# Optimization experiments

Measured on AMD Instinct MI355X. Metric: run time of the kernel, lower is better.

Reference implementation:

```python
import jax, jax.numpy as jnp
import numpy as np

N_NODES = 100000
N_EDGES = 1600000
N_GRAPHS = 512
IN_FEATS = 128
HIDDEN = 128
EXTRA = 8


def setup_inputs() -> dict:
    key = jax.random.key(0)
    ks = jax.random.split(key, 20)
    inp = {
        'feats_node': jax.random.normal(ks[0], (N_NODES, IN_FEATS), jnp.float32),
        'feats_graph': jax.random.normal(ks[1], (N_GRAPHS, EXTRA), jnp.float32),
        'edge_src': jax.random.randint(ks[2], (N_EDGES,), 0, N_NODES, jnp.int32),
        'edge_dst': jax.random.randint(ks[3], (N_EDGES,), 0, N_NODES, jnp.int32),
        'graph_ids': jnp.sort(jax.random.randint(ks[4], (N_NODES,), 0, N_GRAPHS, jnp.int32)),
        # GraphConv weights (in, out) and biases, init ~ N(0, 0.5^2) / zeros as in torch code
        'W1': 0.5 * jax.random.normal(ks[5], (IN_FEATS, HIDDEN), jnp.float32),
        'b1': jnp.zeros((HIDDEN,), jnp.float32),
        'W2': 0.5 * jax.random.normal(ks[6], (HIDDEN, HIDDEN), jnp.float32),
        'b2': jnp.zeros((HIDDEN,), jnp.float32),
        'W3': 0.5 * jax.random.normal(ks[7], (HIDDEN, HIDDEN), jnp.float32),
        'b3': jnp.zeros((HIDDEN,), jnp.float32),
        # MLP head
        'Wl1': 0.5 * jax.random.normal(ks[8], (HIDDEN + EXTRA, 2 * HIDDEN), jnp.float32),
        'bl1': jnp.zeros((2 * HIDDEN,), jnp.float32),
        'Wl2': 0.5 * jax.random.normal(ks[9], (2 * HIDDEN, HIDDEN), jnp.float32),
        'bl2': jnp.zeros((HIDDEN,), jnp.float32),
        'Wl3': 0.5 * jax.random.normal(ks[10], (HIDDEN, 1), jnp.float32),
        'bl3': jnp.zeros((1,), jnp.float32),
    }
    return inp


def _graph_conv(x, edge_src, edge_dst, norm_src, norm_dst, W, b):
    # DGL GraphConv, norm='both': D_dst^{-1/2} A D_src^{-1/2} X W + b
    h = x * norm_src[:, None]
    agg = jax.ops.segment_sum(h[edge_src], edge_dst, num_segments=N_NODES)
    agg = agg * norm_dst[:, None]
    return agg @ W + b


def reference(feats_node, feats_graph, edge_src, edge_dst, graph_ids,
              W1, b1, W2, b2, W3, b3, Wl1, bl1, Wl2, bl2, Wl3, bl3):
    ones_e = jnp.ones((N_EDGES,), jnp.float32)
    deg_out = jax.ops.segment_sum(ones_e, edge_src, num_segments=N_NODES)
    deg_in = jax.ops.segment_sum(ones_e, edge_dst, num_segments=N_NODES)
    norm_src = jnp.clip(deg_out, 1.0) ** -0.5  # out-degree norm on source side
    norm_dst = jnp.clip(deg_in, 1.0) ** -0.5   # in-degree norm on dest side

    x = jax.nn.selu(_graph_conv(feats_node, edge_src, edge_dst, norm_src, norm_dst, W1, b1))
    x = jax.nn.selu(_graph_conv(x, edge_src, edge_dst, norm_src, norm_dst, W2, b2))
    x = _graph_conv(x, edge_src, edge_dst, norm_src, norm_dst, W3, b3)

    # segment-mean readout per graph
    sums = jax.ops.segment_sum(x, graph_ids, num_segments=N_GRAPHS)
    counts = jax.ops.segment_sum(jnp.ones((N_NODES,), jnp.float32), graph_ids, num_segments=N_GRAPHS)
    embedding = sums / jnp.clip(counts, 1.0)[:, None]

    y = jnp.concatenate([embedding, feats_graph], axis=1)
    y = jax.nn.selu(y @ Wl1 + bl1)
    y = jax.nn.selu(y @ Wl2 + bl2)
    return (y @ Wl3 + bl3).reshape(-1)
```

## Files before the change

kernel.cpp:

```cpp
#include <hip/hip_runtime.h>
#include <hip/hip_fp16.h>
#include <math.h>

#define N_NODES   100000
#define N_EDGES   1600000
#define N_GRAPHS  512
#define FEAT      128
#define EXTRA     8

#define NB    196
#define CAPB  10240
#define PA_T  3072
#define PA_K  12

typedef _Float16 half8_t __attribute__((ext_vector_type(8)));
typedef float    f32x4_t __attribute__((ext_vector_type(4)));

static __device__ __forceinline__ float selu_f(float x){
    const float alpha = 1.6732632423543772f;
    const float scale = 1.0507009873554805f;
    return scale * (x > 0.0f ? x : alpha * expm1f(x));
}

__global__ void k_initcur(int* __restrict__ gcursor, int* __restrict__ scursor){
    int i = threadIdx.x;
    if (i < NB){ gcursor[i] = i*CAPB; scursor[i] = i*CAPB; }
}

__global__ __launch_bounds__(256) void k_passA2(
        const int* __restrict__ esrc, const int* __restrict__ edst,
        int* __restrict__ gcursor, int* __restrict__ scursor,
        unsigned* __restrict__ tmp, ushort* __restrict__ tmp2){
    __shared__ int      lcount[NB];
    __shared__ int      lscan[256];
    __shared__ int      gbase[NB];
    __shared__ ushort   bid[PA_T];
    __shared__ unsigned staged[PA_T];
    __shared__ int      Vtot;
    int t = threadIdx.x;
    int base = blockIdx.x * PA_T;

    unsigned ed[PA_K], es[PA_K]; int valid[PA_K];
    #pragma unroll
    for (int k = 0; k < PA_K; ++k){
        int e = base + k*256 + t;
        valid[k] = (e < N_EDGES);
        ed[k] = valid[k] ? (unsigned)edst[e] : 0u;
        es[k] = valid[k] ? (unsigned)esrc[e] : 0u;
    }

    for (int i = t; i < NB; i += 256) lcount[i] = 0;
    __syncthreads();
    int bk[PA_K], slot[PA_K];
    #pragma unroll
    for (int k = 0; k < PA_K; ++k){
        if (valid[k]){
            bk[k] = (int)(ed[k] >> 9);
            slot[k] = atomicAdd(&lcount[bk[k]], 1);
        } else bk[k] = -1;
    }
    __syncthreads();
    int v = (t < NB) ? lcount[t] : 0;
    lscan[t] = v;
    __syncthreads();
    for (int d = 1; d < 256; d <<= 1){
        int u = (t >= d) ? lscan[t-d] : 0;
        __syncthreads();
        lscan[t] += u;
        __syncthreads();
    }
    int excl = lscan[t] - v;
    if (t < NB) gbase[t] = atomicAdd(&gcursor[t], v);
    __syncthreads();
    lscan[t] = excl;
    if (t == 255) Vtot = excl + v;
    __syncthreads();
    #pragma unroll
    for (int k = 0; k < PA_K; ++k){
        if (bk[k] >= 0){
            int i = lscan[bk[k]] + slot[k];
            staged[i] = (ed[k] & 511u) | (es[k] << 9);
            bid[i] = (ushort)bk[k];
        }
    }
    __syncthreads();
    {
        int total = Vtot;
        for (int i = t; i < total; i += 256){
            int b = bid[i];
            tmp[gbase[b] + (i - lscan[b])] = staged[i];
        }
    }
    __syncthreads();

    ushort* sstag = (ushort*)staged;
    for (int i = t; i < NB; i += 256) lcount[i] = 0;
    __syncthreads();
    #pragma unroll
    for (int k = 0; k < PA_K; ++k){
        if (valid[k]){
            bk[k] = (int)(es[k] >> 9);
            slot[k] = atomicAdd(&lcount[bk[k]], 1);
        } else bk[k] = -1;
    }
    __syncthreads();
    v = (t < NB) ? lcount[t] : 0;
    lscan[t] = v;
    __syncthreads();
    for (int d = 1; d < 256; d <<= 1){
        int u = (t >= d) ? lscan[t-d] : 0;
        __syncthreads();
        lscan[t] += u;
        __syncthreads();
    }
    excl = lscan[t] - v;
    if (t < NB) gbase[t] = atomicAdd(&scursor[t], v);
    __syncthreads();
    lscan[t] = excl;
    if (t == 255) Vtot = excl + v;
    __syncthreads();
    #pragma unroll
    for (int k = 0; k < PA_K; ++k){
        if (bk[k] >= 0){
            int i = lscan[bk[k]] + slot[k];
            sstag[i] = (ushort)(es[k] & 511u);
            bid[i] = (ushort)bk[k];
        }
    }
    __syncthreads();
    {
        int total = Vtot;
        for (int i = t; i < total; i += 256){
            int b = bid[i];
            tmp2[gbase[b] + (i - lscan[b])] = sstag[i];
        }
    }
}

__global__ __launch_bounds__(256) void k_srchist(
        const ushort* __restrict__ tmp2, const int* __restrict__ scursor,
        float* __restrict__ ns){
    __shared__ int hc[512];
    int b = blockIdx.x, t = threadIdx.x;
    int node0 = b << 9;
    int lo = b*CAPB;
    int hi = scursor[b]; if (hi > lo + CAPB) hi = lo + CAPB;
    hc[t] = 0; hc[t+256] = 0;
    __syncthreads();
    for (int p = lo + t; p < hi; p += 256)
        atomicAdd(&hc[tmp2[p]], 1);
    __syncthreads();
    int n0 = node0 + t, n1 = n0 + 256;
    if (n0 < N_NODES){ int c = hc[t];     ns[n0] = rsqrtf((float)(c > 1 ? c : 1)); }
    if (n1 < N_NODES){ int c = hc[t+256]; ns[n1] = rsqrtf((float)(c > 1 ? c : 1)); }
}

__global__ __launch_bounds__(256) void k_passB(
        const unsigned* __restrict__ tmp, const int* __restrict__ gcursor,
        int* __restrict__ row_beg, int* __restrict__ row_end,
        int* __restrict__ col, float* __restrict__ nd){
    __shared__ int hc[512];
    __shared__ int hs[512];
    int b = blockIdx.x, t = threadIdx.x;
    int node0 = b << 9;
    int lo = b*CAPB;
    int hi = gcursor[b]; if (hi > lo + CAPB) hi = lo + CAPB;
    hc[t] = 0; hc[t+256] = 0;
    __syncthreads();
    for (int p = lo + t; p < hi; p += 256)
        atomicAdd(&hc[tmp[p] & 511u], 1);
    __syncthreads();
    int a0 = hc[2*t], a1 = hc[2*t+1];
    int s = a0 + a1;
    hs[t] = s;
    __syncthreads();
    for (int d = 1; d < 256; d <<= 1){
        int u = (t >= d) ? hs[t-d] : 0;
        __syncthreads();
        hs[t] += u;
        __syncthreads();
    }
    int excl = hs[t] - s;
    __syncthreads();
    hs[2*t]   = excl;
    hs[2*t+1] = excl + a0;
    int n0 = node0 + 2*t, n1 = n0 + 1;
    if (n0 < N_NODES){
        row_beg[n0] = lo + excl;
        row_end[n0] = lo + excl + a0;
        nd[n0] = rsqrtf((float)(a0 > 1 ? a0 : 1));
    }
    if (n1 < N_NODES){
        row_beg[n1] = lo + excl + a0;
        row_end[n1] = lo + excl + a0 + a1;
        nd[n1] = rsqrtf((float)(a1 > 1 ? a1 : 1));
    }
    __syncthreads();
    for (int p = lo + t; p < hi; p += 256){
        unsigned e = tmp[p];
        int slot = atomicAdd(&hs[e & 511u], 1);
        col[lo + slot] = (int)((e >> 9) << 8);
    }
}

__global__ void k_prep(const float2* __restrict__ x2, const float* __restrict__ ns,
                       __half2* __restrict__ xh2){
    int i = blockIdx.x*blockDim.x + threadIdx.x;
    if (i < N_NODES*64){
        int node = i >> 6;
        float w = ns[node];
        float2 v = x2[i];
        xh2[i] = __floats2half2_rn(v.x*w, v.y*w);
    }
}

__global__ void k_wprep2(const float* __restrict__ W1, __half* __restrict__ Wf1,
                         const float* __restrict__ W2, __half* __restrict__ Wf2){
    int gi = blockIdx.x*256 + threadIdx.x;
    const float* W  = (gi < 16384) ? W1 : W2;
    __half* Wf      = (gi < 16384) ? Wf1 : Wf2;
    int i = gi & 16383;
    int j = i & 7, lane = (i>>3) & 63, kk = (i>>9) & 3, c = i>>11;
    int k = kk*32 + ((lane>>4)<<3) + j;
    int cc = (c<<4) + (lane & 15);
    Wf[i] = __float2half(W[k*FEAT + cc]);
}

__global__ __launch_bounds__(1024, 8) void k_agg_gemm(
        const __half* __restrict__ xh_in, const int* __restrict__ row_beg,
        const int* __restrict__ row_end, const int* __restrict__ col,
        const float* __restrict__ nd, const __half* __restrict__ Wf,
        const float* __restrict__ bias, const float* __restrict__ ns,
        __half* __restrict__ xh_out){
    __shared__ __half Xl[16][136];
    int w = threadIdx.x >> 6, lane = threadIdx.x & 63;
    int sub = lane >> 4, fl = lane & 15;
    int nb0 = blockIdx.x * 16;
    int node = nb0 + w;
    {
        int beg = row_beg[node], end = row_end[node];
        const char* base = (const char*)xh_in + fl*16;
        __half2 acc[4];
        #pragma unroll
        for (int q = 0; q < 4; ++q) acc[q] = __floats2half2_rn(0.f, 0.f);
        for (int eb = beg; eb < end; eb += 16){
            int off[4];
            uint4 r[4];
            #pragma unroll
            for (int j = 0; j < 4; ++j){
                int e = eb + 4*j + sub;
                off[j] = (e < end) ? col[e] : -1;
            }
            #pragma unroll
            for (int j = 0; j < 4; ++j){
                r[j] = (off[j] >= 0)
                     ? *(const uint4*)(base + off[j])
                     : make_uint4(0u,0u,0u,0u);
            }
            #pragma unroll
            for (int j = 0; j < 4; ++j){
                const __half2* h = (const __half2*)&r[j];
                #pragma unroll
                for (int q = 0; q < 4; ++q)
                    acc[q] = __hadd2(acc[q], h[q]);
            }
        }
        #pragma unroll
        for (int q = 0; q < 4; ++q){
            union { __half2 h; int i; } u2, v2;
            u2.h = acc[q];
            v2.i = __shfl_xor(u2.i, 16, 64);
            u2.h = __hadd2(u2.h, v2.h);
            v2.i = __shfl_xor(u2.i, 32, 64);
            acc[q] = __hadd2(u2.h, v2.h);
        }
        if (lane < 16){
            float wd = nd[node];
            union { __half2 h[4]; uint4 u; } pk;
            #pragma unroll
            for (int q = 0; q < 4; ++q){
                float2 f = __half22float2(acc[q]);
                pk.h[q] = __floats2half2_rn(f.x*wd, f.y*wd);
            }
            *(uint4*)&Xl[w][fl*8] = pk.u;
        }
    }
    __syncthreads();
    if (w < 8){
        int rl = lane & 15, kg = lane >> 4;
        half8_t a[4];
        #pragma unroll
        for (int kk = 0; kk < 4; ++kk)
            a[kk] = *(const half8_t*)&Xl[rl][kg*8 + kk*32];
        const half8_t* Bf = (const half8_t*)Wf;
        f32x4_t acc = (f32x4_t){0.f,0.f,0.f,0.f};
        #pragma unroll
        for (int kk = 0; kk < 4; ++kk)
            acc = __builtin_amdgcn_mfma_f32_16x16x32_f16(a[kk], Bf[(w*4+kk)*64+lane], acc, 0, 0, 0);
        int orow0 = nb0 + kg*4;
        int ccol = w*16 + rl;
        float bv = bias[ccol];
        #pragma unroll
        for (int r = 0; r < 4; ++r){
            int orow = orow0 + r;
            float v = acc[r] + bv;
            v = selu_f(v);
            xh_out[(size_t)orow*FEAT + ccol] = __float2half(v * ns[orow]);
        }
    }
}

__global__ __launch_bounds__(256) void k_aggregate_h(
        const __half* __restrict__ xh, const int* __restrict__ row_beg,
        const int* __restrict__ row_end, const int* __restrict__ col,
        const float* __restrict__ nd, __half* __restrict__ outh){
    int gid  = blockIdx.x*blockDim.x + threadIdx.x;
    int node = gid >> 6;
    if (node >= N_NODES) return;
    int lane = threadIdx.x & 63;
    int sub  = lane >> 4;
    int fl   = lane & 15;
    int beg = row_beg[node], end = row_end[node];
    const char* base = (const char*)xh + fl*16;

    __half2 acc[4];
    #pragma unroll
    for (int q = 0; q < 4; ++q) acc[q] = __floats2half2_rn(0.f, 0.f);

    for (int eb = beg; eb < end; eb += 16){
        int off[4];
        uint4 r[4];
        #pragma unroll
        for (int j = 0; j < 4; ++j){
            int e = eb + 4*j + sub;
            off[j] = (e < end) ? col[e] : -1;
        }
        #pragma unroll
        for (int j = 0; j < 4; ++j){
            r[j] = (off[j] >= 0)
                 ? *(const uint4*)(base + off[j])
                 : make_uint4(0u,0u,0u,0u);
        }
        #pragma unroll
        for (int j = 0; j < 4; ++j){
            const __half2* h = (const __half2*)&r[j];
            #pragma unroll
            for (int q = 0; q < 4; ++q)
                acc[q] = __hadd2(acc[q], h[q]);
        }
    }
    #pragma unroll
    for (int q = 0; q < 4; ++q){
        union { __half2 h; int i; } u, v;
        u.h = acc[q];
        v.i = __shfl_xor(u.i, 16, 64);
        u.h = __hadd2(u.h, v.h);
        v.i = __shfl_xor(u.i, 32, 64);
        acc[q] = __hadd2(u.h, v.h);
    }
    if (lane < 16){
        float wd = nd[node];
        union { __half2 h[4]; uint4 u; } pk;
        #pragma unroll
        for (int q = 0; q < 4; ++q){
            float2 f = __half22float2(acc[q]);
            pk.h[q] = __floats2half2_rn(f.x*wd, f.y*wd);
        }
        *(uint4*)(outh + (size_t)node*FEAT + fl*8) = pk.u;
    }
}

__global__ void k_goff(const int* __restrict__ gid, int* __restrict__ goff){
    int g = blockIdx.x*blockDim.x + threadIdx.x;
    if (g > N_GRAPHS) return;
    if (g == N_GRAPHS){ goff[g] = N_NODES; return; }
    int lo = 0, hi = N_NODES;
    while (lo < hi){
        int mid = (lo + hi) >> 1;
        if (gid[mid] < g) lo = mid + 1; else hi = mid;
    }
    goff[g] = lo;
}

__global__ __launch_bounds__(256) void k_readout_h(
        const __half* __restrict__ ah, const int* __restrict__ goff,
        float* __restrict__ emb_part){
    __shared__ float red[16][FEAT];
    int g = blockIdx.x >> 2, c = blockIdx.x & 3;
    int t = threadIdx.x;
    int fl = t & 15, rs = t >> 4;
    int beg = goff[g], end = goff[g+1];
    int cnt = end - beg;
    int chunk = (cnt + 3) >> 2;
    int lo = beg + c*chunk;
    int hi = lo + chunk; if (hi > end) hi = end;
    float acc[8] = {0,0,0,0,0,0,0,0};
    for (int r = lo + rs; r < hi; r += 16){
        uint4 v = *(const uint4*)(ah + (size_t)r*FEAT + fl*8);
        const __half2* h = (const __half2*)&v;
        #pragma unroll
        for (int q = 0; q < 4; ++q){
            float2 f = __half22float2(h[q]);
            acc[2*q]   += f.x;
            acc[2*q+1] += f.y;
        }
    }
    #pragma unroll
    for (int q = 0; q < 8; ++q) red[rs][fl*8+q] = acc[q];
    __syncthreads();
    if (t < FEAT){
        float s = 0.f;
        #pragma unroll
        for (int i = 0; i < 16; ++i) s += red[i][t];
        emb_part[((size_t)g*4 + c)*FEAT + t] = s;
    }
}

__global__ __launch_bounds__(256) void k_mlp(
        const float* __restrict__ emb_part, const int* __restrict__ goff,
        const float* __restrict__ fg,
        const float* __restrict__ W3, const float* __restrict__ b3,
        const float* __restrict__ Wl1, const float* __restrict__ bl1,
        const float* __restrict__ Wl2, const float* __restrict__ bl2,
        const float* __restrict__ Wl3, const float* __restrict__ bl3,
        float* __restrict__ out){
    __shared__ float e[FEAT];
    __shared__ float in136[FEAT+EXTRA];
    __shared__ float y1[256];
    __shared__ float y2[128];
    int g = blockIdx.x, t = threadIdx.x;
    int cnt = goff[g+1] - goff[g]; if (cnt < 1) cnt = 1;
    float inv = 1.f / (float)cnt;
    if (t < FEAT){
        const float* p = emb_part + (size_t)g*4*FEAT;
        e[t] = (p[t] + p[FEAT+t] + p[2*FEAT+t] + p[3*FEAT+t]) * inv;
    }
    __syncthreads();
    if (t < FEAT){
        float acc = b3[t];
        for (int i = 0; i < FEAT; ++i) acc += e[i] * W3[i*FEAT + t];
        in136[t] = acc;
    } else if (t < FEAT+EXTRA){
        in136[t] = fg[g*EXTRA + (t-FEAT)];
    }
    __syncthreads();
    {
        float acc = bl1[t];
        for (int i = 0; i < FEAT+EXTRA; ++i) acc += in136[i] * Wl1[i*256 + t];
        y1[t] = selu_f(acc);
    }
    __syncthreads();
    if (t < 128){
        float acc = bl2[t];
        for (int i = 0; i < 256; ++i) acc += y1[i] * Wl2[i*128 + t];
        y2[t] = selu_f(acc);
    }
    __syncthreads();
    if (t == 0){
        float s = bl3[0];
        for (int i = 0; i < 128; ++i) s += y2[i] * Wl3[i];
        out[g] = s;
    }
}

extern "C" void kernel_launch(void* const* d_in, const int* in_sizes, int n_in,
                              void* d_out, int out_size, void* d_ws, size_t ws_size,
                              hipStream_t stream){
    const float* feats_node  = (const float*)d_in[0];
    const float* feats_graph = (const float*)d_in[1];
    const int*   edge_src    = (const int*)d_in[2];
    const int*   edge_dst    = (const int*)d_in[3];
    const int*   graph_ids   = (const int*)d_in[4];
    const float* W1 =(const float*)d_in[5];  const float* b1 =(const float*)d_in[6];
    const float* W2 =(const float*)d_in[7];  const float* b2 =(const float*)d_in[8];
    const float* W3 =(const float*)d_in[9];  const float* b3 =(const float*)d_in[10];
    const float* Wl1=(const float*)d_in[11]; const float* bl1=(const float*)d_in[12];
    const float* Wl2=(const float*)d_in[13]; const float* bl2=(const float*)d_in[14];
    const float* Wl3=(const float*)d_in[15]; const float* bl3=(const float*)d_in[16];
    float* out = (float*)d_out;
    (void)in_sizes; (void)n_in; (void)out_size; (void)ws_size;

    char* ws = (char*)d_ws;
    size_t off = 0;
    auto alloc = [&](size_t bytes)->void*{
        void* p = ws + off;
        off += (bytes + 255) & ~(size_t)255;
        return p;
    };
    __half*   xhA     = (__half*)  alloc((size_t)N_NODES*FEAT*2);
    __half*   xhB     = (__half*)  alloc((size_t)N_NODES*FEAT*2);
    __half*   ah      = (__half*)  alloc((size_t)N_NODES*FEAT*2);
    float*    ns      = (float*)   alloc((size_t)N_NODES*4);
    float*    nd      = (float*)   alloc((size_t)N_NODES*4);
    int*      row_beg = (int*)     alloc((size_t)N_NODES*4);
    int*      row_end = (int*)     alloc((size_t)N_NODES*4);
    int*      col     = (int*)     alloc((size_t)NB*CAPB*4);
    unsigned* tmp     = (unsigned*)alloc((size_t)NB*CAPB*4);
    ushort*   tmp2    = (ushort*)  alloc((size_t)NB*CAPB*2);
    int*      gcursor = (int*)     alloc((size_t)NB*4);
    int*      scursor = (int*)     alloc((size_t)NB*4);
    __half*   Wf1     = (__half*)  alloc((size_t)16384*2);
    __half*   Wf2     = (__half*)  alloc((size_t)16384*2);
    int*      goff    = (int*)     alloc((size_t)(N_GRAPHS+1)*4);
    float*    emb_part= (float*)   alloc((size_t)N_GRAPHS*4*FEAT*4);

    k_initcur<<<dim3(1), dim3(256), 0, stream>>>(gcursor, scursor);
    k_passA2<<<dim3((N_EDGES + PA_T - 1)/PA_T), dim3(256), 0, stream>>>(
        edge_src, edge_dst, gcursor, scursor, tmp, tmp2);
    k_passB<<<dim3(NB), dim3(256), 0, stream>>>(tmp, gcursor, row_beg, row_end, col, nd);
    k_srchist<<<dim3(NB), dim3(256), 0, stream>>>(tmp2, scursor, ns);

    k_wprep2<<<dim3(128), dim3(256), 0, stream>>>(W1, Wf1, W2, Wf2);

    k_prep<<<dim3((N_NODES*64 + 255)/256), dim3(256), 0, stream>>>(
        (const float2*)feats_node, ns, (__half2*)xhA);

    k_goff<<<dim3((N_GRAPHS+1+255)/256), dim3(256), 0, stream>>>(graph_ids, goff);

    dim3 fusedGrid(N_NODES/16);
    dim3 aggGrid((N_NODES*64 + 255)/256);
    k_agg_gemm<<<fusedGrid, dim3(1024), 0, stream>>>(
        xhA, row_beg, row_end, col, nd, Wf1, b1, ns, xhB);
    k_agg_gemm<<<fusedGrid, dim3(1024), 0, stream>>>(
        xhB, row_beg, row_end, col, nd, Wf2, b2, ns, xhA);
    k_aggregate_h<<<aggGrid, dim3(256), 0, stream>>>(xhA, row_beg, row_end, col, nd, ah);

    k_readout_h<<<dim3(N_GRAPHS*4), dim3(256), 0, stream>>>(ah, goff, emb_part);
    k_mlp<<<dim3(N_GRAPHS), dim3(256), 0, stream>>>(emb_part, goff, feats_graph,
        W3, b3, Wl1, bl1, Wl2, bl2, Wl3, bl3, out);
}
```

Before: 323.9 us.

## Sort nodes by in-degree to balance warps in fused aggregate-GEMM kernel

Adds a degree histogram, a scan and a scatter that build a permutation of nodes grouped by in-degree (capped at 63). The fused aggregation+GEMM kernel then gives each 16-node block nodes of similar degree, so the wavefronts in a block finish their gathers at about the same time before the shared MFMA stage. This costs three extra small kernel launches, and output rows are now written to scattered node indices rather than contiguous ones, which loses some locality in the gathers and stores.

Result: slower. 341.2 us (+5.3%).

```diff
diff --git a/kernel.cpp b/kernel.cpp
--- a/kernel.cpp
+++ b/kernel.cpp
@@ -22,9 +22,11 @@
     return scale * (x > 0.0f ? x : alpha * expm1f(x));
 }
 
-__global__ void k_initcur(int* __restrict__ gcursor, int* __restrict__ scursor){
+__global__ void k_initcur(int* __restrict__ gcursor, int* __restrict__ scursor,
+                          int* __restrict__ dhist){
     int i = threadIdx.x;
     if (i < NB){ gcursor[i] = i*CAPB; scursor[i] = i*CAPB; }
+    if (i < 64) dhist[i] = 0;
 }
 
 __global__ __launch_bounds__(256) void k_passA2(
@@ -203,6 +205,55 @@
     }
 }
 
+__global__ __launch_bounds__(256) void k_dhist(
+        const int* __restrict__ rb, const int* __restrict__ re,
+        int* __restrict__ dh){
+    __shared__ int lh[64];
+    for (int i = threadIdx.x; i < 64; i += 256) lh[i] = 0;
+    __syncthreads();
+    int stride = gridDim.x*blockDim.x;
+    for (int n = blockIdx.x*blockDim.x + threadIdx.x; n < N_NODES; n += stride){
+        int d = re[n] - rb[n]; if (d > 63) d = 63;
+        atomicAdd(&lh[d], 1);
+    }
+    __syncthreads();
+    for (int i = threadIdx.x; i < 64; i += 256)
+        if (lh[i]) atomicAdd(&dh[i], lh[i]);
+}
+
+__global__ void k_dscan(const int* __restrict__ dh, int* __restrict__ dcur){
+    if (threadIdx.x == 0 && blockIdx.x == 0){
+        int run = 0;
+        for (int i = 0; i < 64; ++i){ dcur[i] = run; run += dh[i]; }
+    }
+}
+
+__global__ __launch_bounds__(256) void k_dscatter(
+        const int* __restrict__ rb, const int* __restrict__ re,
+        int* __restrict__ dcur, int* __restrict__ perm){
+    __shared__ int cnt[64];
+    __shared__ int gb[64];
+    int t = threadIdx.x, n0 = blockIdx.x*1024;
+    for (int i = t; i < 64; i += 256) cnt[i] = 0;
+    __syncthreads();
+    int bin[4], slot[4];
+    #pragma unroll
+    for (int k = 0; k < 4; ++k){
+        int n = n0 + k*256 + t;
+        if (n < N_NODES){
+            int d = re[n] - rb[n]; if (d > 63) d = 63;
+            bin[k] = d;
+            slot[k] = atomicAdd(&cnt[d], 1);
+        } else bin[k] = -1;
+    }
+    __syncthreads();
+    if (t < 64) gb[t] = cnt[t] ? atomicAdd(&dcur[t], cnt[t]) : 0;
+    __syncthreads();
+    #pragma unroll
+    for (int k = 0; k < 4; ++k)
+        if (bin[k] >= 0) perm[gb[bin[k]] + slot[k]] = n0 + k*256 + t;
+}
+
 __global__ void k_prep(const float2* __restrict__ x2, const float* __restrict__ ns,
                        __half2* __restrict__ xh2){
     int i = blockIdx.x*blockDim.x + threadIdx.x;
@@ -227,16 +278,17 @@
 }
 
 __global__ __launch_bounds__(1024, 8) void k_agg_gemm(
-        const __half* __restrict__ xh_in, const int* __restrict__ row_beg,
-        const int* __restrict__ row_end, const int* __restrict__ col,
-        const float* __restrict__ nd, const __half* __restrict__ Wf,
-        const float* __restrict__ bias, const float* __restrict__ ns,
-        __half* __restrict__ xh_out){
+        const __half* __restrict__ xh_in, const int* __restrict__ perm,
+        const int* __restrict__ row_beg, const int* __restrict__ row_end,
+        const int* __restrict__ col, const float* __restrict__ nd,
+        const __half* __restrict__ Wf, const float* __restrict__ bias,
+        const float* __restrict__ ns, __half* __restrict__ xh_out){
     __shared__ __half Xl[16][136];
+    __shared__ int nid[16];
     int w = threadIdx.x >> 6, lane = threadIdx.x & 63;
     int sub = lane >> 4, fl = lane & 15;
-    int nb0 = blockIdx.x * 16;
-    int node = nb0 + w;
+    int node = perm[blockIdx.x*16 + w];
+    if (lane == 0) nid[w] = node;
     {
         int beg = row_beg[node], end = row_end[node];
         const char* base = (const char*)xh_in + fl*16;
@@ -297,12 +349,11 @@
         #pragma unroll
         for (int kk = 0; kk < 4; ++kk)
             acc = __builtin_amdgcn_mfma_f32_16x16x32_f16(a[kk], Bf[(w*4+kk)*64+lane], acc, 0, 0, 0);
-        int orow0 = nb0 + kg*4;
         int ccol = w*16 + rl;
         float bv = bias[ccol];
         #pragma unroll
         for (int r = 0; r < 4; ++r){
-            int orow = orow0 + r;
+            int orow = nid[kg*4 + r];
             float v = acc[r] + bv;
             v = selu_f(v);
             xh_out[(size_t)orow*FEAT + ccol] = __float2half(v * ns[orow]);
@@ -494,22 +545,30 @@
     float*    nd      = (float*)   alloc((size_t)N_NODES*4);
     int*      row_beg = (int*)     alloc((size_t)N_NODES*4);
     int*      row_end = (int*)     alloc((size_t)N_NODES*4);
+    int*      perm    = (int*)     alloc((size_t)N_NODES*4);
     int*      col     = (int*)     alloc((size_t)NB*CAPB*4);
     unsigned* tmp     = (unsigned*)alloc((size_t)NB*CAPB*4);
     ushort*   tmp2    = (ushort*)  alloc((size_t)NB*CAPB*2);
     int*      gcursor = (int*)     alloc((size_t)NB*4);
     int*      scursor = (int*)     alloc((size_t)NB*4);
+    int*      dhist   = (int*)     alloc((size_t)64*4);
+    int*      dcur    = (int*)     alloc((size_t)64*4);
     __half*   Wf1     = (__half*)  alloc((size_t)16384*2);
     __half*   Wf2     = (__half*)  alloc((size_t)16384*2);
     int*      goff    = (int*)     alloc((size_t)(N_GRAPHS+1)*4);
     float*    emb_part= (float*)   alloc((size_t)N_GRAPHS*4*FEAT*4);
 
-    k_initcur<<<dim3(1), dim3(256), 0, stream>>>(gcursor, scursor);
+    k_initcur<<<dim3(1), dim3(256), 0, stream>>>(gcursor, scursor, dhist);
     k_passA2<<<dim3((N_EDGES + PA_T - 1)/PA_T), dim3(256), 0, stream>>>(
         edge_src, edge_dst, gcursor, scursor, tmp, tmp2);
     k_passB<<<dim3(NB), dim3(256), 0, stream>>>(tmp, gcursor, row_beg, row_end, col, nd);
     k_srchist<<<dim3(NB), dim3(256), 0, stream>>>(tmp2, scursor, ns);
 
+    k_dhist<<<dim3(392), dim3(256), 0, stream>>>(row_beg, row_end, dhist);
+    k_dscan<<<dim3(1), dim3(64), 0, stream>>>(dhist, dcur);
+    k_dscatter<<<dim3((N_NODES + 1023)/1024), dim3(256), 0, stream>>>(
+        row_beg, row_end, dcur, perm);
+
     k_wprep2<<<dim3(128), dim3(256), 0, stream>>>(W1, Wf1, W2, Wf2);
 
     k_prep<<<dim3((N_NODES*64 + 255)/256), dim3(256), 0, stream>>>(
@@ -520,9 +579,9 @@
     dim3 fusedGrid(N_NODES/16);
     dim3 aggGrid((N_NODES*64 + 255)/256);
     k_agg_gemm<<<fusedGrid, dim3(1024), 0, stream>>>(
-        xhA, row_beg, row_end, col, nd, Wf1, b1, ns, xhB);
+        xhA, perm, row_beg, row_end, col, nd, Wf1, b1, ns, xhB);
     k_agg_gemm<<<fusedGrid, dim3(1024), 0, stream>>>(
-        xhB, row_beg, row_end, col, nd, Wf2, b2, ns, xhA);
+        xhB, perm, row_beg, row_end, col, nd, Wf2, b2, ns, xhA);
     k_aggregate_h<<<aggGrid, dim3(256), 0, stream>>>(xhA, row_beg, row_end, col, nd, ah);
 
     k_readout_h<<<dim3(N_GRAPHS*4), dim3(256), 0, stream>>>(ah, goff, emb_part);
```

## Make fused aggregate-GEMM per-wave with register-shuffled MFMA operands, no LDS

Applied to the files above, without the earlier changes.

Replaces the 1024-thread, 16-node-per-block fused aggregation+GEMM kernel with a 256-thread kernel where each wave handles one node on its own. The aggregated row is broadcast into MFMA A operands with shuffles, only one of the 16 rows is non-zero, and eight 16x16x32 MFMA chains compute all 128 outputs. This drops the block-wide barrier, the LDS staging and the idle-wave imbalance from varying degrees. In exchange it issues about 16x more MFMA work per node and wastes most of it on zero rows.

Result: slower. 506.6 us (+56.4%).

```diff
diff --git a/kernel.cpp b/kernel.cpp
--- a/kernel.cpp
+++ b/kernel.cpp
@@ -226,86 +226,93 @@
     Wf[i] = __float2half(W[k*FEAT + cc]);
 }
 
-__global__ __launch_bounds__(1024, 8) void k_agg_gemm(
+__global__ __launch_bounds__(256) void k_agg_gemm_w(
         const __half* __restrict__ xh_in, const int* __restrict__ row_beg,
         const int* __restrict__ row_end, const int* __restrict__ col,
         const float* __restrict__ nd, const __half* __restrict__ Wf,
         const float* __restrict__ bias, const float* __restrict__ ns,
         __half* __restrict__ xh_out){
-    __shared__ __half Xl[16][136];
-    int w = threadIdx.x >> 6, lane = threadIdx.x & 63;
-    int sub = lane >> 4, fl = lane & 15;
-    int nb0 = blockIdx.x * 16;
-    int node = nb0 + w;
-    {
-        int beg = row_beg[node], end = row_end[node];
-        const char* base = (const char*)xh_in + fl*16;
-        __half2 acc[4];
-        #pragma unroll
-        for (int q = 0; q < 4; ++q) acc[q] = __floats2half2_rn(0.f, 0.f);
-        for (int eb = beg; eb < end; eb += 16){
-            int off[4];
-            uint4 r[4];
+    int gid  = blockIdx.x*blockDim.x + threadIdx.x;
+    int node = gid >> 6;
+    if (node >= N_NODES) return;
+    int lane = threadIdx.x & 63;
+    int sub  = lane >> 4;
+    int fl   = lane & 15;
+    int beg = row_beg[node], end = row_end[node];
+    const char* base = (const char*)xh_in + fl*16;
+
+    __half2 acc[4];
+    #pragma unroll
+    for (int q = 0; q < 4; ++q) acc[q] = __floats2half2_rn(0.f, 0.f);
+    for (int eb = beg; eb < end; eb += 16){
+        int off[4];
+        uint4 r[4];
+        #pragma unroll
+        for (int j = 0; j < 4; ++j){
+            int e = eb + 4*j + sub;
+            off[j] = (e < end) ? col[e] : -1;
+        }
+        #pragma unroll
+        for (int j = 0; j < 4; ++j){
+            r[j] = (off[j] >= 0)
+                 ? *(const uint4*)(base + off[j])
+                 : make_uint4(0u,0u,0u,0u);
+        }
+        #pragma unroll
+        for (int j = 0; j < 4; ++j){
+            const __half2* h = (const __half2*)&r[j];
             #pragma unroll
-            for (int j = 0; j < 4; ++j){
-                int e = eb + 4*j + sub;
-                off[j] = (e < end) ? col[e] : -1;
-            }
-            #pragma unroll
-            for (int j = 0; j < 4; ++j){
-                r[j] = (off[j] >= 0)
-                     ? *(const uint4*)(base + off[j])
-                     : make_uint4(0u,0u,0u,0u);
-            }
-            #pragma unroll
-            for (int j = 0; j < 4; ++j){
-                const __half2* h = (const __half2*)&r[j];
-                #pragma unroll
-                for (int q = 0; q < 4; ++q)
-                    acc[q] = __hadd2(acc[q], h[q]);
-            }
-        }
+            for (int q = 0; q < 4; ++q)
+                acc[q] = __hadd2(acc[q], h[q]);
+        }
+    }
+    #pragma unroll
+    for (int q = 0; q < 4; ++q){
+        union { __half2 h; int i; } u, v;
+        u.h = acc[q];
+        v.i = __shfl_xor(u.i, 16, 64);
+        u.h = __hadd2(u.h, v.h);
+        v.i = __shfl_xor(u.i, 32, 64);
+        acc[q] = __hadd2(u.h, v.h);
+    }
+    float wd = nd[node];
+    __half2 wdh = __floats2half2_rn(wd, wd);
+    int Xw[4];
+    #pragma unroll
+    for (int q = 0; q < 4; ++q){
+        union { __half2 h; int u; } tx;
+        tx.h = __hmul2(acc[q], wdh);
+        Xw[q] = tx.u;
+    }
+    half8_t a[4];
+    #pragma unroll
+    for (int kk = 0; kk < 4; ++kk){
+        int g = kk*4 + sub;
+        union { int u[4]; half8_t v; } A;
         #pragma unroll
         for (int q = 0; q < 4; ++q){
-            union { __half2 h; int i; } u2, v2;
-            u2.h = acc[q];
-            v2.i = __shfl_xor(u2.i, 16, 64);
-            u2.h = __hadd2(u2.h, v2.h);
-            v2.i = __shfl_xor(u2.i, 32, 64);
-            acc[q] = __hadd2(u2.h, v2.h);
-        }
-        if (lane < 16){
-            float wd = nd[node];
-            union { __half2 h[4]; uint4 u; } pk;
-            #pragma unroll
-            for (int q = 0; q < 4; ++q){
-                float2 f = __half22float2(acc[q]);
-                pk.h[q] = __floats2half2_rn(f.x*wd, f.y*wd);
-            }
-            *(uint4*)&Xl[w][fl*8] = pk.u;
-        }
-    }
-    __syncthreads();
-    if (w < 8){
-        int rl = lane & 15, kg = lane >> 4;
-        half8_t a[4];
+            int w = __shfl(Xw[q], g, 64);
+            A.u[q] = (fl == 0) ? w : 0;
+        }
+        a[kk] = A.v;
+    }
+    const half8_t* Bf = (const half8_t*)Wf;
+    float outv[8];
+    #pragma unroll
+    for (int c = 0; c < 8; ++c){
+        f32x4_t ca = (f32x4_t){0.f,0.f,0.f,0.f};
         #pragma unroll
         for (int kk = 0; kk < 4; ++kk)
-            a[kk] = *(const half8_t*)&Xl[rl][kg*8 + kk*32];
-        const half8_t* Bf = (const half8_t*)Wf;
-        f32x4_t acc = (f32x4_t){0.f,0.f,0.f,0.f};
-        #pragma unroll
-        for (int kk = 0; kk < 4; ++kk)
-            acc = __builtin_amdgcn_mfma_f32_16x16x32_f16(a[kk], Bf[(w*4+kk)*64+lane], acc, 0, 0, 0);
-        int orow0 = nb0 + kg*4;
-        int ccol = w*16 + rl;
-        float bv = bias[ccol];
-        #pragma unroll
-        for (int r = 0; r < 4; ++r){
-            int orow = orow0 + r;
-            float v = acc[r] + bv;
+            ca = __builtin_amdgcn_mfma_f32_16x16x32_f16(a[kk], Bf[(c*4+kk)*64 + lane], ca, 0, 0, 0);
+        outv[c] = ca[0];
+    }
+    if (lane < 16){
+        float nsv = ns[node];
+        #pragma unroll
+        for (int c = 0; c < 8; ++c){
+            float v = outv[c] + bias[c*16 + lane];
             v = selu_f(v);
-            xh_out[(size_t)orow*FEAT + ccol] = __float2half(v * ns[orow]);
+            xh_out[(size_t)node*FEAT + c*16 + lane] = __float2half(v * nsv);
         }
     }
 }
@@ -517,11 +524,10 @@
 
     k_goff<<<dim3((N_GRAPHS+1+255)/256), dim3(256), 0, stream>>>(graph_ids, goff);
 
-    dim3 fusedGrid(N_NODES/16);
     dim3 aggGrid((N_NODES*64 + 255)/256);
-    k_agg_gemm<<<fusedGrid, dim3(1024), 0, stream>>>(
+    k_agg_gemm_w<<<aggGrid, dim3(256), 0, stream>>>(
         xhA, row_beg, row_end, col, nd, Wf1, b1, ns, xhB);
-    k_agg_gemm<<<fusedGrid, dim3(1024), 0, stream>>>(
+    k_agg_gemm_w<<<aggGrid, dim3(256), 0, stream>>>(
         xhB, row_beg, row_end, col, nd, Wf2, b2, ns, xhA);
     k_aggregate_h<<<aggGrid, dim3(256), 0, stream>>>(xhA, row_beg, row_end, col, nd, ah);
 
```

## Sort nodes by in-degree within 512-node chunks to balance fused agg-GEMM blocks

Applied to the files above, without the earlier changes.

Adds a kernel that builds a per-chunk permutation of nodes bucketed by in-degree, so each 16-node block of the fused aggregate+GEMM kernel handles nodes of similar degree. The fused kernel reads node ids through this permutation and scatters its output rows to the permuted ids held in shared memory. The aim is to cut wave imbalance, where a block waits for its highest-degree node before the shared MFMA stage. In exchange it adds an extra launch, an indirection per node and scattered output writes that lose the contiguous row order.

Measured after the change: 354.6 us. 1.09x slower.

```diff
diff --git a/kernel.cpp b/kernel.cpp
--- a/kernel.cpp
+++ b/kernel.cpp
@@ -203,6 +203,37 @@
     }
 }
 
+__global__ __launch_bounds__(256) void k_bsort(
+        const int* __restrict__ rb, const int* __restrict__ re,
+        int* __restrict__ perm){
+    __shared__ int h[64];
+    __shared__ int bo[64];
+    int b = blockIdx.x, t = threadIdx.x;
+    int n0 = b << 9;
+    int nend = n0 + 512; if (nend > N_NODES) nend = N_NODES;
+    for (int i = t; i < 64; i += 256) h[i] = 0;
+    __syncthreads();
+    int bin[2], slot[2];
+    #pragma unroll
+    for (int k = 0; k < 2; ++k){
+        int n = n0 + k*256 + t;
+        if (n < nend){
+            int d = re[n] - rb[n]; if (d > 63) d = 63;
+            bin[k] = d;
+            slot[k] = atomicAdd(&h[d], 1);
+        } else bin[k] = -1;
+    }
+    __syncthreads();
+    if (t == 0){
+        int run = 0;
+        for (int i = 0; i < 64; ++i){ bo[i] = run; run += h[i]; }
+    }
+    __syncthreads();
+    #pragma unroll
+    for (int k = 0; k < 2; ++k)
+        if (bin[k] >= 0) perm[n0 + bo[bin[k]] + slot[k]] = n0 + k*256 + t;
+}
+
 __global__ void k_prep(const float2* __restrict__ x2, const float* __restrict__ ns,
                        __half2* __restrict__ xh2){
     int i = blockIdx.x*blockDim.x + threadIdx.x;
@@ -227,16 +258,17 @@
 }
 
 __global__ __launch_bounds__(1024, 8) void k_agg_gemm(
-        const __half* __restrict__ xh_in, const int* __restrict__ row_beg,
-        const int* __restrict__ row_end, const int* __restrict__ col,
-        const float* __restrict__ nd, const __half* __restrict__ Wf,
-        const float* __restrict__ bias, const float* __restrict__ ns,
-        __half* __restrict__ xh_out){
+        const __half* __restrict__ xh_in, const int* __restrict__ perm,
+        const int* __restrict__ row_beg, const int* __restrict__ row_end,
+        const int* __restrict__ col, const float* __restrict__ nd,
+        const __half* __restrict__ Wf, const float* __restrict__ bias,
+        const float* __restrict__ ns, __half* __restrict__ xh_out){
     __shared__ __half Xl[16][136];
+    __shared__ int nid[16];
     int w = threadIdx.x >> 6, lane = threadIdx.x & 63;
     int sub = lane >> 4, fl = lane & 15;
-    int nb0 = blockIdx.x * 16;
-    int node = nb0 + w;
+    int node = perm[blockIdx.x*16 + w];
+    if (lane == 0) nid[w] = node;
     {
         int beg = row_beg[node], end = row_end[node];
         const char* base = (const char*)xh_in + fl*16;
@@ -297,12 +329,11 @@
         #pragma unroll
         for (int kk = 0; kk < 4; ++kk)
             acc = __builtin_amdgcn_mfma_f32_16x16x32_f16(a[kk], Bf[(w*4+kk)*64+lane], acc, 0, 0, 0);
-        int orow0 = nb0 + kg*4;
         int ccol = w*16 + rl;
         float bv = bias[ccol];
         #pragma unroll
         for (int r = 0; r < 4; ++r){
-            int orow = orow0 + r;
+            int orow = nid[kg*4 + r];
             float v = acc[r] + bv;
             v = selu_f(v);
             xh_out[(size_t)orow*FEAT + ccol] = __float2half(v * ns[orow]);
@@ -494,6 +525,7 @@
     float*    nd      = (float*)   alloc((size_t)N_NODES*4);
     int*      row_beg = (int*)     alloc((size_t)N_NODES*4);
     int*      row_end = (int*)     alloc((size_t)N_NODES*4);
+    int*      perm    = (int*)     alloc((size_t)N_NODES*4);
     int*      col     = (int*)     alloc((size_t)NB*CAPB*4);
     unsigned* tmp     = (unsigned*)alloc((size_t)NB*CAPB*4);
     ushort*   tmp2    = (ushort*)  alloc((size_t)NB*CAPB*2);
@@ -510,6 +542,8 @@
     k_passB<<<dim3(NB), dim3(256), 0, stream>>>(tmp, gcursor, row_beg, row_end, col, nd);
     k_srchist<<<dim3(NB), dim3(256), 0, stream>>>(tmp2, scursor, ns);
 
+    k_bsort<<<dim3(NB), dim3(256), 0, stream>>>(row_beg, row_end, perm);
+
     k_wprep2<<<dim3(128), dim3(256), 0, stream>>>(W1, Wf1, W2, Wf2);
 
     k_prep<<<dim3((N_NODES*64 + 255)/256), dim3(256), 0, stream>>>(
@@ -520,9 +554,9 @@
     dim3 fusedGrid(N_NODES/16);
     dim3 aggGrid((N_NODES*64 + 255)/256);
     k_agg_gemm<<<fusedGrid, dim3(1024), 0, stream>>>(
-        xhA, row_beg, row_end, col, nd, Wf1, b1, ns, xhB);
+        xhA, perm, row_beg, row_end, col, nd, Wf1, b1, ns, xhB);
     k_agg_gemm<<<fusedGrid, dim3(1024), 0, stream>>>(
-        xhB, row_beg, row_end, col, nd, Wf2, b2, ns, xhA);
+        xhB, perm, row_beg, row_end, col, nd, Wf2, b2, ns, xhA);
     k_aggregate_h<<<aggGrid, dim3(256), 0, stream>>>(xhA, row_beg, row_end, col, nd, ah);
 
     k_readout_h<<<dim3(N_GRAPHS*4), dim3(256), 0, stream>>>(ah, goff, emb_part);
```
